# Kernel tuning notes

Measured on AMD Instinct MI355X. Metric: run time of the kernel, lower is better.

## Reference

```python
import jax, jax.numpy as jnp
import numpy as np

T, L, C = 256, 32, 8
B, D = 16, 512


def _content_matrix(T, L, C):
    # Faithful port of compute_content_matrix: binary indicator (L, L, C, T).
    # Only upper-triangular (i <= j) window pairs are populated.
    Wc = np.zeros((L, L, C, T), dtype=np.float32)
    stride = T // L
    for i in range(L):
        for j in range(i, L):
            window_size = j - i + 1
            window_start = i * stride
            num_frames = window_size * stride
            clip_size = num_frames // C if num_frames > C else 1
            for c in range(min(C, num_frames)):
                clip_start = window_start + c * clip_size
                Wc[i, j, c, clip_start:clip_start + clip_size] = 1.0
    return Wc


def setup_inputs() -> dict:
    key = jax.random.key(0)
    f = jax.random.normal(key, (B, T, D), dtype=jnp.float32)
    Wc = jnp.asarray(_content_matrix(T, L, C))
    return {"f": f, "Wc": Wc}


def reference(f, Wc):
    # fc[b,l,m,c,d] = sum_t Wc[l,m,c,t] * f[b,t,d]  -> clip content features
    fc = jnp.einsum('lmct,btd->blmcd', Wc, f)  # (B, L, L, C, D)
    # fm: sum over clips within each window
    fm = jnp.sum(fc, axis=3)  # (B, L, L, D)
    # NOTE: original torch code overwrites the avg-pooled tensor with a fresh
    # permute of f, so fb is just f transposed (the pooling result is discarded).
    fb = jnp.transpose(f, (0, 2, 1))  # (B, D, T)
    return fc, fm, fb
```

## Files before the change

### kernel.cpp

```cpp
#include <hip/hip_runtime.h>

#define TT 256
#define LL 32
#define CC 8
#define BB 16
#define DD 512
#define D4 (DD / 4)
#define NCHUNK 16
#define CHUNK 16

#define FC_ELEMS ((long)BB * LL * LL * CC * DD)
#define FM_ELEMS ((long)BB * LL * LL * DD)
#define FM_OFF   FC_ELEMS
#define FB_OFF   (FC_ELEMS + FM_ELEMS)

#define CSUM_FLOATS ((long)BB * NCHUNK * DD)
#define S_ROWS      (TT + 1)
#define S_OFF_FLOATS CSUM_FLOATS

__device__ __forceinline__ float4 f4add(float4 a, float4 b) {
  return make_float4(a.x + b.x, a.y + b.y, a.z + b.z, a.w + b.w);
}
__device__ __forceinline__ float4 f4sub(float4 a, float4 b) {
  return make_float4(a.x - b.x, a.y - b.y, a.z - b.z, a.w - b.w);
}

__global__ __launch_bounds__(256) void chunk_sum_kernel(
    const float4* __restrict__ f4, float4* __restrict__ csum4) {
  int tid = blockIdx.x * blockDim.x + threadIdx.x;
  int d4 = tid & (D4 - 1);
  int chunk = (tid >> 7) & (NCHUNK - 1);
  int b = tid >> 11;
  const float4* fp = f4 + (long)(b * TT + chunk * CHUNK) * D4 + d4;
  float4 s = make_float4(0.f, 0.f, 0.f, 0.f);
#pragma unroll
  for (int i = 0; i < CHUNK; ++i) s = f4add(s, fp[(long)i * D4]);
  csum4[tid] = s;
}

__global__ __launch_bounds__(256) void scan_kernel(
    const float4* __restrict__ f4, const float4* __restrict__ csum4,
    float4* __restrict__ S4, float4* __restrict__ fb4) {
  int tid = blockIdx.x * blockDim.x + threadIdx.x;
  int d4 = tid & (D4 - 1);
  int chunk = (tid >> 7) & (NCHUNK - 1);
  int b = tid >> 11;

  const float4* cp = csum4 + (long)b * NCHUNK * D4 + d4;
  float4 acc = make_float4(0.f, 0.f, 0.f, 0.f);
  for (int i = 0; i < chunk; ++i) acc = f4add(acc, cp[(long)i * D4]);

  const float4* fp = f4 + (long)(b * TT + chunk * CHUNK) * D4 + d4;
  float4* Sp = S4 + ((long)b * S_ROWS + chunk * CHUNK) * D4 + d4;
  if (chunk == 0) Sp[0] = make_float4(0.f, 0.f, 0.f, 0.f);

  float4 vals[CHUNK];
#pragma unroll
  for (int i = 0; i < CHUNK; ++i) {
    vals[i] = fp[(long)i * D4];
    acc = f4add(acc, vals[i]);
    Sp[(long)(i + 1) * D4] = acc;
  }

  const float* v = (const float*)vals;
#pragma unroll
  for (int dd = 0; dd < 4; ++dd) {
    float4* fbp = fb4 + ((long)(b * DD + 4 * d4 + dd) * TT + chunk * CHUNK) / 4;
#pragma unroll
    for (int j = 0; j < 4; ++j) {
      fbp[j] = make_float4(v[(4 * j + 0) * 4 + dd], v[(4 * j + 1) * 4 + dd],
                           v[(4 * j + 2) * 4 + dd], v[(4 * j + 3) * 4 + dd]);
    }
  }
}

__global__ __launch_bounds__(128) void fc_fm_kernel(
    const float* __restrict__ S, float* __restrict__ out) {
  int i = blockIdx.x;
  int vblk = ((i & 7) << 11) | (i >> 3);
  int b = vblk >> 10;
  int l = (vblk >> 5) & (LL - 1);
  int m = vblk & (LL - 1);
  int d4 = threadIdx.x;

  float4* outv = (float4*)out;
  long blm = (long)((b * LL + l) * LL + m);
  long fc_base = blm * CC * D4;
  long fm_base = FM_OFF / 4 + blm * D4;

  if (l > m) {
    float4 z = make_float4(0.f, 0.f, 0.f, 0.f);
#pragma unroll
    for (int c = 0; c < CC; ++c) outv[fc_base + (long)c * D4 + d4] = z;
    outv[fm_base + d4] = z;
    return;
  }

  int w = m - l + 1;
  const float4* S4 = (const float4*)S;
  long srow = (long)b * S_ROWS;

  float4 s[9];
#pragma unroll
  for (int c = 0; c <= 8; ++c) {
    int p = 8 * l + c * w;
    s[c] = S4[(srow + p) * D4 + d4];
  }

#pragma unroll
  for (int c = 0; c < CC; ++c)
    outv[fc_base + (long)c * D4 + d4] = f4sub(s[c + 1], s[c]);
  outv[fm_base + d4] = f4sub(s[8], s[0]);
}

extern "C" void kernel_launch(void* const* d_in, const int* in_sizes, int n_in,
                              void* d_out, int out_size, void* d_ws, size_t ws_size,
                              hipStream_t stream) {
  const float4* f4 = (const float4*)d_in[0];
  float* out = (float*)d_out;

  float4* csum4 = (float4*)d_ws;
  float4* S4 = (float4*)((float*)d_ws + S_OFF_FLOATS);
  float4* fb4 = (float4*)(out + FB_OFF);

  {
    int total4 = BB * NCHUNK * D4;
    chunk_sum_kernel<<<total4 / 256, 256, 0, stream>>>(f4, csum4);
    scan_kernel<<<total4 / 256, 256, 0, stream>>>(f4, csum4, S4, fb4);
  }
  {
    fc_fm_kernel<<<BB * LL * LL, 128, 0, stream>>>((const float*)S4, out);
  }
}
```

Baseline: 322.7 us.

## Fuse chunk-sum and scan into one block-scan kernel; use nontemporal output stores

Replaces the two-pass prefix-sum (chunk sums then scan) with a single kernel that computes chunk partials in shared memory and scans within a block, removing one launch and the workspace round trip. Also switches all large output writes (fc, fm, fb) to nontemporal stores to reduce cache pollution on the write-bandwidth-bound streams. Nontemporal hints may behave differently on this hardware and could hurt write combining.

```diff
diff --git a/kernel.cpp b/kernel.cpp
--- a/kernel.cpp
+++ b/kernel.cpp
@@ -6,17 +6,17 @@
 #define BB 16
 #define DD 512
 #define D4 (DD / 4)
-#define NCHUNK 16
-#define CHUNK 16
 
 #define FC_ELEMS ((long)BB * LL * LL * CC * DD)
 #define FM_ELEMS ((long)BB * LL * LL * DD)
 #define FM_OFF   FC_ELEMS
 #define FB_OFF   (FC_ELEMS + FM_ELEMS)
 
-#define CSUM_FLOATS ((long)BB * NCHUNK * DD)
-#define S_ROWS      (TT + 1)
-#define S_OFF_FLOATS CSUM_FLOATS
+#define S_ROWS   (TT + 1)
+
+#define SCHUNK   8
+#define NSCHUNK  (TT / SCHUNK)
+#define D4PB     8
 
 __device__ __forceinline__ float4 f4add(float4 a, float4 b) {
   return make_float4(a.x + b.x, a.y + b.y, a.z + b.z, a.w + b.w);
@@ -25,39 +25,42 @@
   return make_float4(a.x - b.x, a.y - b.y, a.z - b.z, a.w - b.w);
 }
 
-__global__ __launch_bounds__(256) void chunk_sum_kernel(
-    const float4* __restrict__ f4, float4* __restrict__ csum4) {
-  int tid = blockIdx.x * blockDim.x + threadIdx.x;
-  int d4 = tid & (D4 - 1);
-  int chunk = (tid >> 7) & (NCHUNK - 1);
-  int b = tid >> 11;
-  const float4* fp = f4 + (long)(b * TT + chunk * CHUNK) * D4 + d4;
+typedef float nf4 __attribute__((ext_vector_type(4)));
+__device__ __forceinline__ void ntstore(float4* p, float4 v) {
+  nf4 nv;
+  nv.x = v.x; nv.y = v.y; nv.z = v.z; nv.w = v.w;
+  __builtin_nontemporal_store(nv, (nf4*)p);
+}
+
+__global__ __launch_bounds__(256) void scan_fb_kernel(
+    const float4* __restrict__ f4, float4* __restrict__ S4,
+    float4* __restrict__ fb4) {
+  __shared__ float4 part[NSCHUNK][D4PB];
+
+  int b = blockIdx.x >> 4;
+  int d4blk = blockIdx.x & 15;
+  int d4local = threadIdx.x & (D4PB - 1);
+  int chunk = threadIdx.x >> 3;
+  int d4 = d4blk * D4PB + d4local;
+
+  const float4* fp = f4 + ((long)(b * TT + chunk * SCHUNK)) * D4 + d4;
+  float4 vals[SCHUNK];
   float4 s = make_float4(0.f, 0.f, 0.f, 0.f);
 #pragma unroll
-  for (int i = 0; i < CHUNK; ++i) s = f4add(s, fp[(long)i * D4]);
-  csum4[tid] = s;
-}
+  for (int i = 0; i < SCHUNK; ++i) {
+    vals[i] = fp[(long)i * D4];
+    s = f4add(s, vals[i]);
+  }
+  part[chunk][d4local] = s;
+  __syncthreads();
 
-__global__ __launch_bounds__(256) void scan_kernel(
-    const float4* __restrict__ f4, const float4* __restrict__ csum4,
-    float4* __restrict__ S4, float4* __restrict__ fb4) {
-  int tid = blockIdx.x * blockDim.x + threadIdx.x;
-  int d4 = tid & (D4 - 1);
-  int chunk = (tid >> 7) & (NCHUNK - 1);
-  int b = tid >> 11;
+  float4 acc = make_float4(0.f, 0.f, 0.f, 0.f);
+  for (int j = 0; j < chunk; ++j) acc = f4add(acc, part[j][d4local]);
 
-  const float4* cp = csum4 + (long)b * NCHUNK * D4 + d4;
-  float4 acc = make_float4(0.f, 0.f, 0.f, 0.f);
-  for (int i = 0; i < chunk; ++i) acc = f4add(acc, cp[(long)i * D4]);
-
-  const float4* fp = f4 + (long)(b * TT + chunk * CHUNK) * D4 + d4;
-  float4* Sp = S4 + ((long)b * S_ROWS + chunk * CHUNK) * D4 + d4;
+  float4* Sp = S4 + ((long)b * S_ROWS + chunk * SCHUNK) * D4 + d4;
   if (chunk == 0) Sp[0] = make_float4(0.f, 0.f, 0.f, 0.f);
-
-  float4 vals[CHUNK];
 #pragma unroll
-  for (int i = 0; i < CHUNK; ++i) {
-    vals[i] = fp[(long)i * D4];
+  for (int i = 0; i < SCHUNK; ++i) {
     acc = f4add(acc, vals[i]);
     Sp[(long)(i + 1) * D4] = acc;
   }
@@ -65,11 +68,12 @@
   const float* v = (const float*)vals;
 #pragma unroll
   for (int dd = 0; dd < 4; ++dd) {
-    float4* fbp = fb4 + ((long)(b * DD + 4 * d4 + dd) * TT + chunk * CHUNK) / 4;
+    float4* fbp = fb4 + (long)(b * DD + 4 * d4 + dd) * (TT / 4) + chunk * 2;
 #pragma unroll
-    for (int j = 0; j < 4; ++j) {
-      fbp[j] = make_float4(v[(4 * j + 0) * 4 + dd], v[(4 * j + 1) * 4 + dd],
-                           v[(4 * j + 2) * 4 + dd], v[(4 * j + 3) * 4 + dd]);
+    for (int j = 0; j < 2; ++j) {
+      float4 t = make_float4(v[(4 * j + 0) * 4 + dd], v[(4 * j + 1) * 4 + dd],
+                             v[(4 * j + 2) * 4 + dd], v[(4 * j + 3) * 4 + dd]);
+      ntstore(&fbp[j], t);
     }
   }
 }
@@ -91,8 +95,8 @@
   if (l > m) {
     float4 z = make_float4(0.f, 0.f, 0.f, 0.f);
 #pragma unroll
-    for (int c = 0; c < CC; ++c) outv[fc_base + (long)c * D4 + d4] = z;
-    outv[fm_base + d4] = z;
+    for (int c = 0; c < CC; ++c) ntstore(&outv[fc_base + (long)c * D4 + d4], z);
+    ntstore(&outv[fm_base + d4], z);
     return;
   }
 
@@ -109,8 +113,8 @@
 
 #pragma unroll
   for (int c = 0; c < CC; ++c)
-    outv[fc_base + (long)c * D4 + d4] = f4sub(s[c + 1], s[c]);
-  outv[fm_base + d4] = f4sub(s[8], s[0]);
+    ntstore(&outv[fc_base + (long)c * D4 + d4], f4sub(s[c + 1], s[c]));
+  ntstore(&outv[fm_base + d4], f4sub(s[8], s[0]));
 }
 
 extern "C" void kernel_launch(void* const* d_in, const int* in_sizes, int n_in,
@@ -119,16 +123,9 @@
   const float4* f4 = (const float4*)d_in[0];
   float* out = (float*)d_out;
 
-  float4* csum4 = (float4*)d_ws;
-  float4* S4 = (float4*)((float*)d_ws + S_OFF_FLOATS);
+  float4* S4 = (float4*)d_ws;
   float4* fb4 = (float4*)(out + FB_OFF);
 
-  {
-    int total4 = BB * NCHUNK * D4;
-    chunk_sum_kernel<<<total4 / 256, 256, 0, stream>>>(f4, csum4);
-    scan_kernel<<<total4 / 256, 256, 0, stream>>>(f4, csum4, S4, fb4);
-  }
-  {
-    fc_fm_kernel<<<BB * LL * LL, 128, 0, stream>>>((const float*)S4, out);
-  }
+  scan_fb_kernel<<<BB * (D4 / D4PB), 256, 0, stream>>>(f4, S4, fb4);
+  fc_fm_kernel<<<BB * LL * LL, 128, 0, stream>>>((const float*)S4, out);
 }
```

Result: no change. 319.1 us (-1.1%).
